# Kernel optimization log

Hardware: AMD Instinct MI355X
Metric: run time of the kernel (lower is better)

## Reference

```python
import jax, jax.numpy as jnp
import numpy as np

T, B, D, H = 2048, 32, 512, 512

def setup_inputs() -> dict:
    key = jax.random.key(0)
    ks = jax.random.split(key, 7)
    stdv = 1.0 / np.sqrt(H)
    return {
        "x": jax.random.normal(ks[0], (T, B, D), dtype=jnp.float32),
        "h0": jax.random.normal(ks[1], (B, H), dtype=jnp.float32),
        "c0": jax.random.normal(ks[2], (B, H), dtype=jnp.float32),
        "w_ih": jax.random.uniform(ks[3], (4 * H, D), jnp.float32, -stdv, stdv),
        "b_ih": jax.random.uniform(ks[4], (4 * H,), jnp.float32, -stdv, stdv),
        "w_hh": jax.random.uniform(ks[5], (4 * H, H), jnp.float32, -stdv, stdv),
        "b_hh": jax.random.uniform(ks[6], (4 * H,), jnp.float32, -stdv, stdv),
    }

def reference(x, h0, c0, w_ih, b_ih, w_hh, b_hh):
    hidden = h0.shape[-1]
    # Precompute input-to-hidden projection for all timesteps: [T, B, 4H]
    gx = jnp.einsum("tbd,gd->tbg", x, w_ih) + b_ih + b_hh

    def step(carry, gx_t):
        h, c = carry
        gates = gx_t + h @ w_hh.T  # [B, 4H]
        i_in, f_in, g_in, o_in = jnp.split(gates, 4, axis=1)
        i_t = jax.nn.sigmoid(i_in)
        f_t = jax.nn.sigmoid(f_in)
        g_t = jnp.tanh(g_in)
        o_t = jax.nn.sigmoid(o_in)
        c_t = f_t * c + i_t * g_t
        h_t = o_t * jnp.tanh(c_t)
        return (h_t, c_t), h_t

    (h_n, c_n), out = jax.lax.scan(step, (h0, c0), gx)
    # out: [T, B, H]; matches DPLSTM output, (h_n, c_n)
    return out, h_n, c_n
```

## Files before the change

### kernel.cpp

```cpp
#include <hip/hip_runtime.h>
#include <hip/hip_bf16.h>

#define T_STEPS 2048
#define BATCH 32
#define DIN 512
#define HID 512
#define G4H 2048
#define NWG 64
#define SLICE 8
#define THREADS 256
#define HPAIRS (BATCH * HID / 2)

typedef __attribute__((ext_vector_type(8))) short short8;
typedef __attribute__((ext_vector_type(4))) float floatx4;
typedef __attribute__((ext_vector_type(4))) unsigned int uintx4;
typedef unsigned long long ull;

__device__ __forceinline__ ushort f2bf(float f) {
  return __builtin_bit_cast(ushort, __float2bfloat16(f));
}

__global__ void prep_kernel(const float* __restrict__ wih, const float* __restrict__ whh,
                            const float* __restrict__ bih, const float* __restrict__ bhh,
                            const float* __restrict__ h0,
                            ushort* __restrict__ wihb, ushort* __restrict__ whhb,
                            float* __restrict__ bias, ull* __restrict__ tagbuf) {
  int i = blockIdx.x * blockDim.x + threadIdx.x;
  const int NW = G4H * DIN;
  if (i < NW) { wihb[i] = f2bf(wih[i]); whhb[i] = f2bf(whh[i]); }
  if (i < G4H) bias[i] = bih[i] + bhh[i];
  if (i < HPAIRS) {
    int b = i >> 8, p = i & 255;
    ull ev = (ull)f2bf(h0[b * HID + 2 * p]);
    ull od = (ull)f2bf(h0[b * HID + 2 * p + 1]);
    tagbuf[i] = (od << 48) | (ev << 32);
    tagbuf[HPAIRS + i] = 0xFFFFFFFFull;
  }
}

__global__ void cvtx_kernel(const float* __restrict__ x, ushort* __restrict__ xb) {
  const size_t N = (size_t)T_STEPS * BATCH * DIN;
  size_t stride = (size_t)gridDim.x * blockDim.x * 4;
  for (size_t idx = ((size_t)blockIdx.x * blockDim.x + threadIdx.x) * 4; idx < N; idx += stride) {
    float4 f = *reinterpret_cast<const float4*>(x + idx);
    ushort4 u;
    u.x = f2bf(f.x); u.y = f2bf(f.y); u.z = f2bf(f.z); u.w = f2bf(f.w);
    *reinterpret_cast<ushort4*>(xb + idx) = u;
  }
}

template <bool XB>
__device__ __forceinline__ floatx4 xpart(const float* __restrict__ x,
                                         const ushort* __restrict__ xb,
                                         int t, int brow, int quad,
                                         const short8* wih_r) {
  floatx4 a = {0.f, 0.f, 0.f, 0.f};
  floatx4 b = {0.f, 0.f, 0.f, 0.f};
  if (XB) {
    const ushort* xt = xb + ((size_t)t * BATCH + brow) * DIN + quad * 8;
#pragma unroll
    for (int kb = 0; kb < 16; ++kb) {
      short8 a0 = *reinterpret_cast<const short8*>(xt + kb * 32);
      if (kb & 1)
        b = __builtin_amdgcn_mfma_f32_16x16x32_bf16(wih_r[kb], a0, b, 0, 0, 0);
      else
        a = __builtin_amdgcn_mfma_f32_16x16x32_bf16(wih_r[kb], a0, a, 0, 0, 0);
    }
  } else {
    const float* xt = x + ((size_t)t * BATCH + brow) * DIN + quad * 8;
#pragma unroll
    for (int kb = 0; kb < 16; ++kb) {
      const float4* xp = reinterpret_cast<const float4*>(xt + kb * 32);
      float4 f0 = xp[0], f1 = xp[1];
      short8 a0;
      a0[0] = (short)f2bf(f0.x); a0[1] = (short)f2bf(f0.y);
      a0[2] = (short)f2bf(f0.z); a0[3] = (short)f2bf(f0.w);
      a0[4] = (short)f2bf(f1.x); a0[5] = (short)f2bf(f1.y);
      a0[6] = (short)f2bf(f1.z); a0[7] = (short)f2bf(f1.w);
      if (kb & 1)
        b = __builtin_amdgcn_mfma_f32_16x16x32_bf16(wih_r[kb], a0, b, 0, 0, 0);
      else
        a = __builtin_amdgcn_mfma_f32_16x16x32_bf16(wih_r[kb], a0, a, 0, 0, 0);
    }
  }
  return a + b;
}

template <bool XB>
__global__ __launch_bounds__(THREADS, 1) void lstm_kernel(
    const float* __restrict__ x, const ushort* __restrict__ xb,
    const float* __restrict__ c0,
    const ushort* __restrict__ wihb, const ushort* __restrict__ whhb,
    const float* __restrict__ bias, ull* __restrict__ tagbuf,
    float* __restrict__ out) {
  const int g = blockIdx.x;
  const int tid = threadIdx.x;
  const int lane = tid & 63;
  const int wave = tid >> 6;
  const int r = wave & 1;
  const int cc = wave >> 1;
  const int n16 = lane & 15;
  const int quad = lane >> 4;
  const int brow = r * 16 + n16;
  const int j = cc * 16 + n16;
  const int wrow = (j & 3) * HID + g * SLICE + (j >> 2);

  const int ecol = g * SLICE + cc * 4 + quad;
  float c_val = c0[brow * HID + ecol];
  const float bi = bias[ecol];
  const float bf_ = bias[HID + ecol];
  const float bg = bias[2 * HID + ecol];
  const float bo = bias[3 * HID + ecol];

  short8 wih_r[16], whh_r[16];
  {
    const ushort* wr = wihb + (size_t)wrow * DIN + quad * 8;
    const ushort* hr = whhb + (size_t)wrow * HID + quad * 8;
#pragma unroll
    for (int kb = 0; kb < 16; ++kb) {
      wih_r[kb] = *reinterpret_cast<const short8*>(wr + kb * 32);
      whh_r[kb] = *reinterpret_cast<const short8*>(hr + kb * 32);
    }
  }

  floatx4 acc0_cur = xpart<XB>(x, xb, 0, brow, quad, wih_r);

  float hlast = 0.f;
  for (int t = 0; t < T_STEPS; ++t) {
    const ull* hb = tagbuf + (size_t)(t & 1) * HPAIRS + (size_t)brow * (HID / 2) + quad * 4;
    const unsigned tagt = (unsigned)t;
    floatx4 acc1a = {0.f, 0.f, 0.f, 0.f};
    floatx4 acc1b = {0.f, 0.f, 0.f, 0.f};
    unsigned done = 0;
    for (;;) {
      ull d[16][4];
#pragma unroll
      for (int kb = 0; kb < 16; ++kb) {
        if (!(done & (1u << kb))) {
#pragma unroll
          for (int m = 0; m < 4; ++m)
            d[kb][m] = __hip_atomic_load(hb + kb * 16 + m, __ATOMIC_RELAXED,
                                         __HIP_MEMORY_SCOPE_AGENT);
        }
      }
#pragma unroll
      for (int kb = 0; kb < 16; ++kb) {
        if (!(done & (1u << kb))) {
          bool ok = ((unsigned)d[kb][0] == tagt) & ((unsigned)d[kb][1] == tagt) &
                    ((unsigned)d[kb][2] == tagt) & ((unsigned)d[kb][3] == tagt);
          if (__all(ok)) {
            uintx4 pk;
            pk.x = (unsigned)(d[kb][0] >> 32);
            pk.y = (unsigned)(d[kb][1] >> 32);
            pk.z = (unsigned)(d[kb][2] >> 32);
            pk.w = (unsigned)(d[kb][3] >> 32);
            short8 hf = __builtin_bit_cast(short8, pk);
            if (kb & 1)
              acc1b = __builtin_amdgcn_mfma_f32_16x16x32_bf16(whh_r[kb], hf, acc1b, 0, 0, 0);
            else
              acc1a = __builtin_amdgcn_mfma_f32_16x16x32_bf16(whh_r[kb], hf, acc1a, 0, 0, 0);
            done |= (1u << kb);
          }
        }
      }
      if (done == 0xFFFFu) break;
      __builtin_amdgcn_s_sleep(1);
    }

    float pi = acc0_cur[0] + acc1a[0] + acc1b[0] + bi;
    float pf = acc0_cur[1] + acc1a[1] + acc1b[1] + bf_;
    float pg = acc0_cur[2] + acc1a[2] + acc1b[2] + bg;
    float po = acc0_cur[3] + acc1a[3] + acc1b[3] + bo;
    float ig = 1.f / (1.f + __expf(-pi));
    float fg = 1.f / (1.f + __expf(-pf));
    float eg = __expf(2.f * pg);
    float gg = 1.f - 2.f / (eg + 1.f);
    float og = 1.f / (1.f + __expf(-po));
    c_val = fg * c_val + ig * gg;
    float ec = __expf(2.f * c_val);
    float tc = 1.f - 2.f / (ec + 1.f);
    float h = og * tc;
    hlast = h;

    unsigned hu = (unsigned)f2bf(h);
    unsigned hpart = (unsigned)__shfl_xor((int)hu, 16);
    if ((quad & 1) == 0) {
      ull v = ((ull)hpart << 48) | ((ull)hu << 32) | (ull)(unsigned)(t + 1);
      ull* dst = tagbuf + (size_t)((t + 1) & 1) * HPAIRS +
                 (size_t)brow * (HID / 2) + (ecol >> 1);
      __hip_atomic_store(dst, v, __ATOMIC_RELAXED, __HIP_MEMORY_SCOPE_AGENT);
    }
    __atomic_signal_fence(__ATOMIC_SEQ_CST);

    float h1 = __shfl_xor(h, 16);
    float h2 = __shfl_xor(h, 32);
    float h3 = __shfl_xor(h1, 32);
    if (quad == 0) {
      float4 o4 = make_float4(h, h1, h2, h3);
      *reinterpret_cast<float4*>(out + (size_t)t * (BATCH * HID) + brow * HID +
                                 g * SLICE + cc * 4) = o4;
    }

    const int tt = (t + 1 < T_STEPS) ? t + 1 : t;
    acc0_cur = xpart<XB>(x, xb, tt, brow, quad, wih_r);
  }
  out[(size_t)T_STEPS * BATCH * HID + brow * HID + ecol] = hlast;
  out[(size_t)T_STEPS * BATCH * HID + BATCH * HID + brow * HID + ecol] = c_val;
}

extern "C" void kernel_launch(void* const* d_in, const int* in_sizes, int n_in,
                              void* d_out, int out_size, void* d_ws, size_t ws_size,
                              hipStream_t stream) {
  const float* x = (const float*)d_in[0];
  const float* h0 = (const float*)d_in[1];
  const float* c0 = (const float*)d_in[2];
  const float* w_ih = (const float*)d_in[3];
  const float* b_ih = (const float*)d_in[4];
  const float* w_hh = (const float*)d_in[5];
  const float* b_hh = (const float*)d_in[6];
  float* out = (float*)d_out;
  char* ws = (char*)d_ws;

  float* bias = (float*)(ws + 1024);
  ushort* wihb = (ushort*)(ws + (16 << 10));
  ushort* whhb = (ushort*)(ws + (16 << 10) + (2 << 20));
  ull* tagbuf = (ull*)(ws + (16 << 10) + (4 << 20));
  ushort* xb = (ushort*)(ws + (8 << 20));
  const size_t xb_bytes = (size_t)T_STEPS * BATCH * DIN * sizeof(ushort);
  const bool use_xb = ws_size >= ((size_t)(8 << 20) + xb_bytes);

  hipLaunchKernelGGL(prep_kernel, dim3(4096), dim3(256), 0, stream,
                     w_ih, w_hh, b_ih, b_hh, h0, wihb, whhb, bias, tagbuf);

  if (use_xb) {
    hipLaunchKernelGGL(cvtx_kernel, dim3(8192), dim3(256), 0, stream, x, xb);
    void* args[] = {(void*)&x, (void*)&xb, (void*)&c0, (void*)&wihb, (void*)&whhb,
                    (void*)&bias, (void*)&tagbuf, (void*)&out};
    hipError_t e = hipLaunchCooperativeKernel(
        reinterpret_cast<void*>(&lstm_kernel<true>), dim3(NWG), dim3(THREADS),
        args, 0, stream);
    if (e != hipSuccess) {
      hipLaunchKernelGGL(lstm_kernel<true>, dim3(NWG), dim3(THREADS), 0, stream,
                         x, xb, c0, wihb, whhb, bias, tagbuf, out);
    }
  } else {
    void* args[] = {(void*)&x, (void*)&xb, (void*)&c0, (void*)&wihb, (void*)&whhb,
                    (void*)&bias, (void*)&tagbuf, (void*)&out};
    hipError_t e = hipLaunchCooperativeKernel(
        reinterpret_cast<void*>(&lstm_kernel<false>), dim3(NWG), dim3(THREADS),
        args, 0, stream);
    if (e != hipSuccess) {
      hipLaunchKernelGGL(lstm_kernel<false>, dim3(NWG), dim3(THREADS), 0, stream,
                         x, xb, c0, wihb, whhb, bias, tagbuf, out);
    }
  }
}
```

Baseline: 23.06 ms.

## Use 16 workgroups with per-block flags and LDS-staged hidden state

Cuts the persistent grid from 64 to 16 workgroups of 512 threads, each covering 32 hidden columns and both 16-row batch halves per wave. Per-element tagged polling of the hidden state is replaced by one flag per workgroup and a monotonic step counter. After the flags are seen, the full bf16 hidden vector is copied into swizzled LDS and consumed by MFMAs. The aim is to cut polling traffic and synchronisation cost per step, at the price of a coarser barrier, an extra LDS round trip and __syncthreads, and fewer CUs doing the per-step work. It relies on relaxed atomics plus the block barrier for memory ordering.

```diff
diff --git a/kernel.cpp b/kernel.cpp
--- a/kernel.cpp
+++ b/kernel.cpp
@@ -6,14 +6,14 @@
 #define DIN 512
 #define HID 512
 #define G4H 2048
-#define NWG 64
-#define SLICE 8
-#define THREADS 256
-#define HPAIRS (BATCH * HID / 2)
+#define NWG 16
+#define SLICE 32
+#define THREADS 512
+#define HU32 (BATCH * HID / 2)
+#define HULL (BATCH * HID / 4)
 
 typedef __attribute__((ext_vector_type(8))) short short8;
 typedef __attribute__((ext_vector_type(4))) float floatx4;
-typedef __attribute__((ext_vector_type(4))) unsigned int uintx4;
 typedef unsigned long long ull;
 
 __device__ __forceinline__ ushort f2bf(float f) {
@@ -24,17 +24,18 @@
                             const float* __restrict__ bih, const float* __restrict__ bhh,
                             const float* __restrict__ h0,
                             ushort* __restrict__ wihb, ushort* __restrict__ whhb,
-                            float* __restrict__ bias, ull* __restrict__ tagbuf) {
+                            float* __restrict__ bias, unsigned* __restrict__ hgu,
+                            unsigned* __restrict__ flags) {
   int i = blockIdx.x * blockDim.x + threadIdx.x;
   const int NW = G4H * DIN;
   if (i < NW) { wihb[i] = f2bf(wih[i]); whhb[i] = f2bf(whh[i]); }
   if (i < G4H) bias[i] = bih[i] + bhh[i];
-  if (i < HPAIRS) {
-    int b = i >> 8, p = i & 255;
-    ull ev = (ull)f2bf(h0[b * HID + 2 * p]);
-    ull od = (ull)f2bf(h0[b * HID + 2 * p + 1]);
-    tagbuf[i] = (od << 48) | (ev << 32);
-    tagbuf[HPAIRS + i] = 0xFFFFFFFFull;
+  if (i < NWG) flags[i] = 0u;
+  if (i < HU32) {
+    int b = i >> 8, cp = i & 255;
+    unsigned lo = f2bf(h0[b * HID + 2 * cp]);
+    unsigned hi = f2bf(h0[b * HID + 2 * cp + 1]);
+    hgu[i] = lo | (hi << 16);
   }
 }
 
@@ -50,40 +51,45 @@
 }
 
 template <bool XB>
-__device__ __forceinline__ floatx4 xpart(const float* __restrict__ x,
-                                         const ushort* __restrict__ xb,
-                                         int t, int brow, int quad,
-                                         const short8* wih_r) {
-  floatx4 a = {0.f, 0.f, 0.f, 0.f};
-  floatx4 b = {0.f, 0.f, 0.f, 0.f};
+__device__ __forceinline__ void xpart2(const float* __restrict__ x,
+                                       const ushort* __restrict__ xb,
+                                       int t, int n16, int quad,
+                                       const short8* wih_r,
+                                       floatx4& o0, floatx4& o1) {
+  floatx4 a0 = {0.f, 0.f, 0.f, 0.f};
+  floatx4 a1 = {0.f, 0.f, 0.f, 0.f};
   if (XB) {
-    const ushort* xt = xb + ((size_t)t * BATCH + brow) * DIN + quad * 8;
+    const ushort* xt0 = xb + ((size_t)t * BATCH + n16) * DIN + quad * 8;
+    const ushort* xt1 = xt0 + 16 * DIN;
 #pragma unroll
     for (int kb = 0; kb < 16; ++kb) {
-      short8 a0 = *reinterpret_cast<const short8*>(xt + kb * 32);
-      if (kb & 1)
-        b = __builtin_amdgcn_mfma_f32_16x16x32_bf16(wih_r[kb], a0, b, 0, 0, 0);
-      else
-        a = __builtin_amdgcn_mfma_f32_16x16x32_bf16(wih_r[kb], a0, a, 0, 0, 0);
+      short8 b0 = *reinterpret_cast<const short8*>(xt0 + kb * 32);
+      short8 b1 = *reinterpret_cast<const short8*>(xt1 + kb * 32);
+      a0 = __builtin_amdgcn_mfma_f32_16x16x32_bf16(wih_r[kb], b0, a0, 0, 0, 0);
+      a1 = __builtin_amdgcn_mfma_f32_16x16x32_bf16(wih_r[kb], b1, a1, 0, 0, 0);
     }
   } else {
-    const float* xt = x + ((size_t)t * BATCH + brow) * DIN + quad * 8;
+    const float* xt0 = x + ((size_t)t * BATCH + n16) * DIN + quad * 8;
+    const float* xt1 = xt0 + 16 * DIN;
 #pragma unroll
     for (int kb = 0; kb < 16; ++kb) {
-      const float4* xp = reinterpret_cast<const float4*>(xt + kb * 32);
-      float4 f0 = xp[0], f1 = xp[1];
-      short8 a0;
-      a0[0] = (short)f2bf(f0.x); a0[1] = (short)f2bf(f0.y);
-      a0[2] = (short)f2bf(f0.z); a0[3] = (short)f2bf(f0.w);
-      a0[4] = (short)f2bf(f1.x); a0[5] = (short)f2bf(f1.y);
-      a0[6] = (short)f2bf(f1.z); a0[7] = (short)f2bf(f1.w);
-      if (kb & 1)
-        b = __builtin_amdgcn_mfma_f32_16x16x32_bf16(wih_r[kb], a0, b, 0, 0, 0);
-      else
-        a = __builtin_amdgcn_mfma_f32_16x16x32_bf16(wih_r[kb], a0, a, 0, 0, 0);
-    }
-  }
-  return a + b;
+      const float4* xp0 = reinterpret_cast<const float4*>(xt0 + kb * 32);
+      const float4* xp1 = reinterpret_cast<const float4*>(xt1 + kb * 32);
+      float4 f0 = xp0[0], f1 = xp0[1], g0 = xp1[0], g1 = xp1[1];
+      short8 b0, b1;
+      b0[0] = (short)f2bf(f0.x); b0[1] = (short)f2bf(f0.y);
+      b0[2] = (short)f2bf(f0.z); b0[3] = (short)f2bf(f0.w);
+      b0[4] = (short)f2bf(f1.x); b0[5] = (short)f2bf(f1.y);
+      b0[6] = (short)f2bf(f1.z); b0[7] = (short)f2bf(f1.w);
+      b1[0] = (short)f2bf(g0.x); b1[1] = (short)f2bf(g0.y);
+      b1[2] = (short)f2bf(g0.z); b1[3] = (short)f2bf(g0.w);
+      b1[4] = (short)f2bf(g1.x); b1[5] = (short)f2bf(g1.y);
+      b1[6] = (short)f2bf(g1.z); b1[7] = (short)f2bf(g1.w);
+      a0 = __builtin_amdgcn_mfma_f32_16x16x32_bf16(wih_r[kb], b0, a0, 0, 0, 0);
+      a1 = __builtin_amdgcn_mfma_f32_16x16x32_bf16(wih_r[kb], b1, a1, 0, 0, 0);
+    }
+  }
+  o0 = a0; o1 = a1;
 }
 
 template <bool XB>
@@ -91,26 +97,24 @@
     const float* __restrict__ x, const ushort* __restrict__ xb,
     const float* __restrict__ c0,
     const ushort* __restrict__ wihb, const ushort* __restrict__ whhb,
-    const float* __restrict__ bias, ull* __restrict__ tagbuf,
-    float* __restrict__ out) {
+    const float* __restrict__ bias, unsigned* __restrict__ hgu,
+    unsigned* __restrict__ flags, float* __restrict__ out) {
   const int g = blockIdx.x;
   const int tid = threadIdx.x;
   const int lane = tid & 63;
   const int wave = tid >> 6;
-  const int r = wave & 1;
-  const int cc = wave >> 1;
   const int n16 = lane & 15;
   const int quad = lane >> 4;
-  const int brow = r * 16 + n16;
-  const int j = cc * 16 + n16;
-  const int wrow = (j & 3) * HID + g * SLICE + (j >> 2);
-
-  const int ecol = g * SLICE + cc * 4 + quad;
-  float c_val = c0[brow * HID + ecol];
-  const float bi = bias[ecol];
-  const float bf_ = bias[HID + ecol];
-  const float bg = bias[2 * HID + ecol];
-  const float bo = bias[3 * HID + ecol];
+
+  const int wrow = (n16 & 3) * HID + g * SLICE + wave * 4 + (n16 >> 2);
+  const int ecol = g * SLICE + wave * 4 + quad;
+
+  float c_v0 = c0[n16 * HID + ecol];
+  float c_v1 = c0[(16 + n16) * HID + ecol];
+  const float b_i = bias[ecol];
+  const float b_f = bias[HID + ecol];
+  const float b_g = bias[2 * HID + ecol];
+  const float b_o = bias[3 * HID + ecol];
 
   short8 wih_r[16], whh_r[16];
   {
@@ -123,89 +127,132 @@
     }
   }
 
-  floatx4 acc0_cur = xpart<XB>(x, xb, 0, brow, quad, wih_r);
-
-  float hlast = 0.f;
+  __shared__ __align__(16) char hlds[2][32 * 1024];
+  const ull* hgq = reinterpret_cast<const ull*>(hgu);
+
+  floatx4 x0, x1;
+  xpart2<XB>(x, xb, 0, n16, quad, wih_r, x0, x1);
+
+  float h_l0 = 0.f, h_l1 = 0.f;
   for (int t = 0; t < T_STEPS; ++t) {
-    const ull* hb = tagbuf + (size_t)(t & 1) * HPAIRS + (size_t)brow * (HID / 2) + quad * 4;
-    const unsigned tagt = (unsigned)t;
-    floatx4 acc1a = {0.f, 0.f, 0.f, 0.f};
-    floatx4 acc1b = {0.f, 0.f, 0.f, 0.f};
-    unsigned done = 0;
-    for (;;) {
-      ull d[16][4];
+    const int par = t & 1;
+    if (t) {
+      const unsigned tgt = (unsigned)t;
+      for (;;) {
+        unsigned f = __hip_atomic_load(&flags[lane & 15], __ATOMIC_RELAXED,
+                                       __HIP_MEMORY_SCOPE_AGENT);
+        if (__all(f >= tgt)) break;
+        __builtin_amdgcn_s_sleep(1);
+      }
+    }
+    __atomic_signal_fence(__ATOMIC_ACQUIRE);
+
+    {
+      const ull* src = hgq + (size_t)par * HULL;
+      ull d[8];
+#pragma unroll
+      for (int m = 0; m < 8; ++m)
+        d[m] = __hip_atomic_load(src + tid + m * 512, __ATOMIC_RELAXED,
+                                 __HIP_MEMORY_SCOPE_AGENT);
+#pragma unroll
+      for (int m = 0; m < 8; ++m) {
+        int jj = tid + m * 512;
+        int row = jj >> 7;
+        int cb = (jj & 127) * 8;
+        *reinterpret_cast<ull*>(&hlds[par][row * 1024 + (cb ^ ((row & 7) << 4))]) = d[m];
+      }
+    }
+    __syncthreads();
+
+    floatx4 a0 = {0.f, 0.f, 0.f, 0.f};
+    floatx4 a1 = {0.f, 0.f, 0.f, 0.f};
+    {
+      const int r0 = n16, r1 = 16 + n16;
+      const int sw0 = (r0 & 7) << 4, sw1 = (r1 & 7) << 4;
 #pragma unroll
       for (int kb = 0; kb < 16; ++kb) {
-        if (!(done & (1u << kb))) {
-#pragma unroll
-          for (int m = 0; m < 4; ++m)
-            d[kb][m] = __hip_atomic_load(hb + kb * 16 + m, __ATOMIC_RELAXED,
-                                         __HIP_MEMORY_SCOPE_AGENT);
-        }
-      }
-#pragma unroll
-      for (int kb = 0; kb < 16; ++kb) {
-        if (!(done & (1u << kb))) {
-          bool ok = ((unsigned)d[kb][0] == tagt) & ((unsigned)d[kb][1] == tagt) &
-                    ((unsigned)d[kb][2] == tagt) & ((unsigned)d[kb][3] == tagt);
-          if (__all(ok)) {
-            uintx4 pk;
-            pk.x = (unsigned)(d[kb][0] >> 32);
-            pk.y = (unsigned)(d[kb][1] >> 32);
-            pk.z = (unsigned)(d[kb][2] >> 32);
-            pk.w = (unsigned)(d[kb][3] >> 32);
-            short8 hf = __builtin_bit_cast(short8, pk);
-            if (kb & 1)
-              acc1b = __builtin_amdgcn_mfma_f32_16x16x32_bf16(whh_r[kb], hf, acc1b, 0, 0, 0);
-            else
-              acc1a = __builtin_amdgcn_mfma_f32_16x16x32_bf16(whh_r[kb], hf, acc1a, 0, 0, 0);
-            done |= (1u << kb);
-          }
-        }
-      }
-      if (done == 0xFFFFu) break;
-      __builtin_amdgcn_s_sleep(1);
-    }
-
-    float pi = acc0_cur[0] + acc1a[0] + acc1b[0] + bi;
-    float pf = acc0_cur[1] + acc1a[1] + acc1b[1] + bf_;
-    float pg = acc0_cur[2] + acc1a[2] + acc1b[2] + bg;
-    float po = acc0_cur[3] + acc1a[3] + acc1b[3] + bo;
-    float ig = 1.f / (1.f + __expf(-pi));
-    float fg = 1.f / (1.f + __expf(-pf));
-    float eg = __expf(2.f * pg);
-    float gg = 1.f - 2.f / (eg + 1.f);
-    float og = 1.f / (1.f + __expf(-po));
-    c_val = fg * c_val + ig * gg;
-    float ec = __expf(2.f * c_val);
-    float tc = 1.f - 2.f / (ec + 1.f);
-    float h = og * tc;
-    hlast = h;
-
-    unsigned hu = (unsigned)f2bf(h);
-    unsigned hpart = (unsigned)__shfl_xor((int)hu, 16);
-    if ((quad & 1) == 0) {
-      ull v = ((ull)hpart << 48) | ((ull)hu << 32) | (ull)(unsigned)(t + 1);
-      ull* dst = tagbuf + (size_t)((t + 1) & 1) * HPAIRS +
-                 (size_t)brow * (HID / 2) + (ecol >> 1);
-      __hip_atomic_store(dst, v, __ATOMIC_RELAXED, __HIP_MEMORY_SCOPE_AGENT);
-    }
-    __atomic_signal_fence(__ATOMIC_SEQ_CST);
-
-    float h1 = __shfl_xor(h, 16);
-    float h2 = __shfl_xor(h, 32);
-    float h3 = __shfl_xor(h1, 32);
-    if (quad == 0) {
-      float4 o4 = make_float4(h, h1, h2, h3);
-      *reinterpret_cast<float4*>(out + (size_t)t * (BATCH * HID) + brow * HID +
-                                 g * SLICE + cc * 4) = o4;
+        int cb = kb * 64 + quad * 16;
+        short8 f0 = *reinterpret_cast<const short8*>(&hlds[par][r0 * 1024 + (cb ^ sw0)]);
+        short8 f1 = *reinterpret_cast<const short8*>(&hlds[par][r1 * 1024 + (cb ^ sw1)]);
+        a0 = __builtin_amdgcn_mfma_f32_16x16x32_bf16(whh_r[kb], f0, a0, 0, 0, 0);
+        a1 = __builtin_amdgcn_mfma_f32_16x16x32_bf16(whh_r[kb], f1, a1, 0, 0, 0);
+      }
+    }
+
+    float h0v, h1v;
+    {
+      float pi = x0[0] + a0[0] + b_i;
+      float pf = x0[1] + a0[1] + b_f;
+      float pg = x0[2] + a0[2] + b_g;
+      float po = x0[3] + a0[3] + b_o;
+      float ig = 1.f / (1.f + __expf(-pi));
+      float fg = 1.f / (1.f + __expf(-pf));
+      float eg = __expf(2.f * pg);
+      float gg = 1.f - 2.f / (eg + 1.f);
+      float og = 1.f / (1.f + __expf(-po));
+      c_v0 = fg * c_v0 + ig * gg;
+      float ec = __expf(2.f * c_v0);
+      h0v = og * (1.f - 2.f / (ec + 1.f));
+    }
+    {
+      float pi = x1[0] + a1[0] + b_i;
+      float pf = x1[1] + a1[1] + b_f;
+      float pg = x1[2] + a1[2] + b_g;
+      float po = x1[3] + a1[3] + b_o;
+      float ig = 1.f / (1.f + __expf(-pi));
+      float fg = 1.f / (1.f + __expf(-pf));
+      float eg = __expf(2.f * pg);
+      float gg = 1.f - 2.f / (eg + 1.f);
+      float og = 1.f / (1.f + __expf(-po));
+      c_v1 = fg * c_v1 + ig * gg;
+      float ec = __expf(2.f * c_v1);
+      h1v = og * (1.f - 2.f / (ec + 1.f));
+    }
+    h_l0 = h0v; h_l1 = h1v;
+
+    const int par1 = par ^ 1;
+    {
+      unsigned hu0 = (unsigned)f2bf(h0v);
+      unsigned hu1 = (unsigned)f2bf(h1v);
+      unsigned hp0 = (unsigned)__shfl_xor((int)hu0, 16);
+      unsigned hp1 = (unsigned)__shfl_xor((int)hu1, 16);
+      if (!(quad & 1)) {
+        unsigned cp = (unsigned)(g * 16 + wave * 2 + (quad >> 1));
+        __hip_atomic_store(&hgu[(size_t)par1 * HU32 + n16 * 256 + cp],
+                           hu0 | (hp0 << 16), __ATOMIC_RELAXED,
+                           __HIP_MEMORY_SCOPE_AGENT);
+        __hip_atomic_store(&hgu[(size_t)par1 * HU32 + (16 + n16) * 256 + cp],
+                           hu1 | (hp1 << 16), __ATOMIC_RELAXED,
+                           __HIP_MEMORY_SCOPE_AGENT);
+      }
+    }
+    __syncthreads();
+    if (tid == 0)
+      __hip_atomic_store(&flags[g], (unsigned)(t + 1), __ATOMIC_RELAXED,
+                         __HIP_MEMORY_SCOPE_AGENT);
+
+    {
+      float u1 = __shfl_xor(h0v, 16), u2 = __shfl_xor(h0v, 32), u3 = __shfl_xor(u1, 32);
+      float v1 = __shfl_xor(h1v, 16), v2 = __shfl_xor(h1v, 32), v3 = __shfl_xor(v1, 32);
+      if (quad == 0) {
+        const int cb = g * SLICE + wave * 4;
+        *reinterpret_cast<float4*>(out + (size_t)t * (BATCH * HID) + n16 * HID + cb) =
+            make_float4(h0v, u1, u2, u3);
+        *reinterpret_cast<float4*>(out + (size_t)t * (BATCH * HID) + (16 + n16) * HID + cb) =
+            make_float4(h1v, v1, v2, v3);
+      }
     }
 
     const int tt = (t + 1 < T_STEPS) ? t + 1 : t;
-    acc0_cur = xpart<XB>(x, xb, tt, brow, quad, wih_r);
-  }
-  out[(size_t)T_STEPS * BATCH * HID + brow * HID + ecol] = hlast;
-  out[(size_t)T_STEPS * BATCH * HID + BATCH * HID + brow * HID + ecol] = c_val;
+    floatx4 xn0, xn1;
+    xpart2<XB>(x, xb, tt, n16, quad, wih_r, xn0, xn1);
+    x0 = xn0; x1 = xn1;
+  }
+
+  out[(size_t)T_STEPS * BATCH * HID + n16 * HID + ecol] = h_l0;
+  out[(size_t)T_STEPS * BATCH * HID + (16 + n16) * HID + ecol] = h_l1;
+  out[(size_t)T_STEPS * BATCH * HID + BATCH * HID + n16 * HID + ecol] = c_v0;
+  out[(size_t)T_STEPS * BATCH * HID + BATCH * HID + (16 + n16) * HID + ecol] = c_v1;
 }
 
 extern "C" void kernel_launch(void* const* d_in, const int* in_sizes, int n_in,
@@ -221,37 +268,38 @@
   float* out = (float*)d_out;
   char* ws = (char*)d_ws;
 
+  unsigned* flags = (unsigned*)ws;
   float* bias = (float*)(ws + 1024);
   ushort* wihb = (ushort*)(ws + (16 << 10));
   ushort* whhb = (ushort*)(ws + (16 << 10) + (2 << 20));
-  ull* tagbuf = (ull*)(ws + (16 << 10) + (4 << 20));
+  unsigned* hgu = (unsigned*)(ws + (16 << 10) + (4 << 20));
   ushort* xb = (ushort*)(ws + (8 << 20));
   const size_t xb_bytes = (size_t)T_STEPS * BATCH * DIN * sizeof(ushort);
   const bool use_xb = ws_size >= ((size_t)(8 << 20) + xb_bytes);
 
   hipLaunchKernelGGL(prep_kernel, dim3(4096), dim3(256), 0, stream,
-                     w_ih, w_hh, b_ih, b_hh, h0, wihb, whhb, bias, tagbuf);
+                     w_ih, w_hh, b_ih, b_hh, h0, wihb, whhb, bias, hgu, flags);
 
   if (use_xb) {
     hipLaunchKernelGGL(cvtx_kernel, dim3(8192), dim3(256), 0, stream, x, xb);
     void* args[] = {(void*)&x, (void*)&xb, (void*)&c0, (void*)&wihb, (void*)&whhb,
-                    (void*)&bias, (void*)&tagbuf, (void*)&out};
+                    (void*)&bias, (void*)&hgu, (void*)&flags, (void*)&out};
     hipError_t e = hipLaunchCooperativeKernel(
         reinterpret_cast<void*>(&lstm_kernel<true>), dim3(NWG), dim3(THREADS),
         args, 0, stream);
     if (e != hipSuccess) {
       hipLaunchKernelGGL(lstm_kernel<true>, dim3(NWG), dim3(THREADS), 0, stream,
-                         x, xb, c0, wihb, whhb, bias, tagbuf, out);
+                         x, xb, c0, wihb, whhb, bias, hgu, flags, out);
     }
   } else {
     void* args[] = {(void*)&x, (void*)&xb, (void*)&c0, (void*)&wihb, (void*)&whhb,
-                    (void*)&bias, (void*)&tagbuf, (void*)&out};
+                    (void*)&bias, (void*)&hgu, (void*)&flags, (void*)&out};
     hipError_t e = hipLaunchCooperativeKernel(
         reinterpret_cast<void*>(&lstm_kernel<false>), dim3(NWG), dim3(THREADS),
         args, 0, stream);
     if (e != hipSuccess) {
       hipLaunchKernelGGL(lstm_kernel<false>, dim3(NWG), dim3(THREADS), 0, stream,
-                         x, xb, c0, wihb, whhb, bias, tagbuf, out);
-    }
-  }
-}
+                         x, xb, c0, wihb, whhb, bias, hgu, flags, out);
+    }
+  }
+}
```

Result: faster. 20.43 ms (-11.4%).
